# Kernel tuning notes

Measured on AMD Instinct MI355X. Metric: run time of the kernel, lower is better.

The kernel has to match this reference:

```python
import jax, jax.numpy as jnp
import numpy as np

H, W, C = 512, 512, 21
D_BI, D_SP = 5, 2
THETA_ALPHA, THETA_BETA, THETA_GAMMA = 80.0, 13.0, 3.0
BILATERAL_COMPAT, SPATIAL_COMPAT, COMPAT = 10.0, 3.0, -1.0
NUM_ITER = 5


def _build_lattice(feats):
    # Permutohedral lattice construction (Adams et al. 2010), vectorized numpy.
    # feats: [N, d] float64 -> (offsets [N,d+1] int32 into M lattice points,
    # barycentric weights [N,d+1] float32, blur_neighbors [d+1, M, 2] int32 (+1, 0=missing)).
    N, d = feats.shape
    scale = (np.sqrt(2.0 / 3.0) * (d + 1)) / np.sqrt((np.arange(d) + 1.0) * (np.arange(d) + 2.0))
    cf = feats * scale                                            # [N, d]
    S = np.concatenate([np.cumsum(cf[:, ::-1], axis=1)[:, ::-1], np.zeros((N, 1))], axis=1)
    elev = np.empty((N, d + 1))
    elev[:, 0] = S[:, 0]
    elev[:, 1:] = S[:, 1:] - np.arange(1, d + 1) * cf             # embed on H_d hyperplane
    rem0 = np.floor(elev / (d + 1) + 0.5) * (d + 1)               # nearest 0-colored point
    sums = np.rint(rem0.sum(1) / (d + 1)).astype(np.int64)
    diff = elev - rem0
    idx = np.arange(d + 1)
    gt = diff[:, None, :] > diff[:, :, None]
    eq = (diff[:, None, :] == diff[:, :, None]) & (idx[None, None, :] < idx[None, :, None])
    rank = (gt | eq).sum(2).astype(np.int64) + sums[:, None]
    lo = rank < 0
    rank += (d + 1) * lo
    rem0 += (d + 1) * lo
    hi = rank > d
    rank -= (d + 1) * hi
    rem0 -= (d + 1) * hi
    v = (elev - rem0) / (d + 1)
    b = np.zeros((N, d + 2))
    rows = np.arange(N)[:, None]
    np.add.at(b, (rows, d - rank), v)
    np.add.at(b, (rows, d + 1 - rank), -v)
    b[:, 0] += 1.0 + b[:, d + 1]
    ws = b[:, :d + 1].astype(np.float32)                          # weight per remainder r
    rem0i = np.rint(rem0[:, :d]).astype(np.int64)
    r = np.arange(d + 1)
    keys = rem0i[:, None, :] + r[None, :, None] - (d + 1) * (rank[:, None, :d] > (d - r)[None, :, None])
    uniq, os_flat = np.unique(keys.reshape(-1, d), axis=0, return_inverse=True)
    M = uniq.shape[0]
    os_ = os_flat.reshape(N, d + 1).astype(np.int32)
    n1 = np.repeat(uniq[None] + 1, d + 1, axis=0)                 # [d+1, M, d]
    n2 = np.repeat(uniq[None] - 1, d + 1, axis=0)
    for j in range(d):
        n1[j, :, j] = uniq[:, j] - d
        n2[j, :, j] = uniq[:, j] + d
    allk = np.concatenate([uniq, n1.reshape(-1, d), n2.reshape(-1, d)], axis=0)
    _, inv = np.unique(allk, axis=0, return_inverse=True)
    lut = np.full(int(inv.max()) + 1, -1, np.int64)
    lut[inv[:M]] = np.arange(M)
    i1 = lut[inv[M:M + (d + 1) * M]].reshape(d + 1, M)
    i2 = lut[inv[M + (d + 1) * M:]].reshape(d + 1, M)
    bn = (np.stack([i1, i2], axis=-1) + 1).astype(np.int32)       # 0 == missing neighbor
    return os_, ws, bn


def setup_inputs():
    key = jax.random.key(0)
    k1, k2 = jax.random.split(key)
    unary = jax.random.normal(k1, (H, W, C), jnp.float32)
    # piecewise-constant random image (realistic local color coherence)
    base = np.asarray(jax.random.uniform(k2, (32, 32, 3)), dtype=np.float64) * 255.0
    image = np.kron(base, np.ones((H // 32, W // 32, 1)))
    yy, xx = np.mgrid[0:H, 0:W].astype(np.float64)
    bi = np.concatenate([np.stack([xx / THETA_ALPHA, yy / THETA_ALPHA], -1),
                         image / THETA_BETA], axis=-1).reshape(-1, D_BI)
    sp = np.stack([xx / THETA_GAMMA, yy / THETA_GAMMA], -1).reshape(-1, D_SP)
    os_b, ws_b, bn_b = _build_lattice(bi)
    os_s, ws_s, bn_s = _build_lattice(sp)
    return {'unary': unary,
            'ws_b': jnp.asarray(ws_b), 'ws_s': jnp.asarray(ws_s),
            'os_b': jnp.asarray(os_b), 'os_s': jnp.asarray(os_s),
            'bn_b': jnp.asarray(bn_b), 'bn_s': jnp.asarray(bn_s)}


def _filter(Q, os_, ws, bn, alpha):
    # splat -> blur -> slice over one permutohedral lattice
    M = bn.shape[1]
    vals = jnp.zeros((M + 1, Q.shape[-1]), Q.dtype)
    vals = vals.at[os_ + 1].add(ws[:, :, None] * Q[:, None, :])   # splat (row 0 = pad)
    for j in range(bn.shape[0]):                                  # blur along d+1 lattice axes
        vals = vals.at[1:].add(0.5 * (vals[bn[j, :, 0]] + vals[bn[j, :, 1]]))
    return alpha * jnp.einsum('nj,njc->nc', ws, vals[os_ + 1])    # slice


def reference(unary, ws_b, ws_s, os_b, os_s, bn_b, bn_s):
    U = unary.reshape(-1, unary.shape[-1])                        # [N, C]
    a_b = 1.0 / (1.0 + 2.0 ** (-D_BI))
    a_s = 1.0 / (1.0 + 2.0 ** (-D_SP))
    ones = jnp.ones((U.shape[0], 1), U.dtype)
    inv_nb = 1.0 / (_filter(ones, os_b, ws_b, bn_b, a_b) + 1e-20)
    inv_ns = 1.0 / (_filter(ones, os_s, ws_s, bn_s, a_s) + 1e-20)
    Q = jax.nn.softmax(-U, axis=-1)
    for _ in range(NUM_ITER):
        msg = BILATERAL_COMPAT * (_filter(Q, os_b, ws_b, bn_b, a_b) * inv_nb) \
            + SPATIAL_COMPAT * (_filter(Q, os_s, ws_s, bn_s, a_s) * inv_ns)
        Q = jax.nn.softmax(-U - COMPAT * msg, axis=-1)
    return Q.reshape(unary.shape)
```

## Files before the change

kernel.cpp:

```cpp
#include <hip/hip_runtime.h>
#include <hip/hip_fp16.h>

#define NCH 21
#define NCH2 22
#define VSH 32
#define QSH 32
#define USH 24
#define NPIX (512*512)
#define SEG 192
#define DECODE (1.0f/(16383.f*128.f))

__device__ __forceinline__ int wave_rank_atomic(int m, bool valid, int* __restrict__ cur) {
  int lane = threadIdx.x & 63;
  unsigned long long todo = __ballot(valid);
  int out = 0;
  while (todo) {
    int leader = __ffsll((unsigned long long)todo) - 1;
    int lm = __shfl(m, leader);
    unsigned long long match = __ballot(valid && (m == lm));
    int cnt = __popcll(match);
    int b = 0;
    if (lane == leader) b = atomicAdd(&cur[lm], cnt);
    b = __shfl(b, leader);
    if (valid && (m == lm)) out = b + __popcll(match & ((1ull << lane) - 1ull));
    todo &= ~match;
  }
  return out;
}


__global__ void count_fused_kernel(const int* __restrict__ os_b, const int* __restrict__ os_s,
                                   int* __restrict__ cnt, int nptot, int Mb) {
  int t = blockIdx.x*blockDim.x + threadIdx.x;
  bool valid = (t < nptot);
  int m = 0;
  if (valid) {
    if (t < 6*NPIX) { int j = t >> 18, n = t & (NPIX-1); m = os_b[n*6+j]; }
    else { int t2 = t - 6*NPIX; int j = t2 >> 18, n = t2 & (NPIX-1); m = Mb + os_s[n*3+j]; }
  }
  int lane = threadIdx.x & 63;
  unsigned long long todo = __ballot(valid);
  while (todo) {
    int leader = __ffsll((unsigned long long)todo) - 1;
    int lm = __shfl(m, leader);
    unsigned long long match = __ballot(valid && (m == lm));
    if (lane == leader) atomicAdd(&cnt[lm], __popcll(match));
    todo &= ~match;
  }
}

__global__ void scan_block_kernel(const int* __restrict__ cnt, int* __restrict__ excl,
                                  int* __restrict__ bsum, int M) {
  __shared__ int s[256];
  int i = blockIdx.x*256 + threadIdx.x;
  int v = (i < M) ? cnt[i] : 0;
  s[threadIdx.x] = v;
  __syncthreads();
  for (int off = 1; off < 256; off <<= 1) {
    int t = (threadIdx.x >= off) ? s[threadIdx.x - off] : 0;
    __syncthreads();
    s[threadIdx.x] += t;
    __syncthreads();
  }
  if (i < M) excl[i] = s[threadIdx.x] - v;
  if (threadIdx.x == 255) bsum[blockIdx.x] = s[255];
}

__global__ void scan_sums_kernel(int* __restrict__ bsum, int nb) {
  __shared__ int s[256];
  __shared__ int carry;
  if (threadIdx.x == 0) carry = 0;
  __syncthreads();
  for (int base = 0; base < nb; base += 256) {
    int i = base + threadIdx.x;
    int v = (i < nb) ? bsum[i] : 0;
    s[threadIdx.x] = v;
    __syncthreads();
    for (int off = 1; off < 256; off <<= 1) {
      int t = (threadIdx.x >= off) ? s[threadIdx.x - off] : 0;
      __syncthreads();
      s[threadIdx.x] += t;
      __syncthreads();
    }
    if (i < nb) bsum[i] = s[threadIdx.x] - v + carry;
    int tot = s[255];
    __syncthreads();
    if (threadIdx.x == 0) carry += tot;
    __syncthreads();
  }
  if (threadIdx.x == 0) bsum[nb] = carry;
}

__global__ void scan_add_kernel(int* __restrict__ excl, const int* __restrict__ bsum,
                                int M, int nb) {
  int i = blockIdx.x*blockDim.x + threadIdx.x;
  if (i < M) excl[i] += bsum[i >> 8];
  else if (i == M) excl[M] = bsum[nb];
}

__global__ void fill_fused_kernel(const int* __restrict__ os_b, const float* __restrict__ ws_b,
                                  const int* __restrict__ os_s, const float* __restrict__ ws_s,
                                  const int* __restrict__ start, int* __restrict__ cur,
                                  unsigned int* __restrict__ pw, int nptot, int Mb) {
  int t = blockIdx.x*blockDim.x + threadIdx.x;
  bool valid = (t < nptot);
  int m = 0, pix = 0; float w = 0.f;
  if (valid) {
    if (t < 6*NPIX) { int j = t >> 18, n = t & (NPIX-1); m = os_b[n*6+j]; pix = n; w = ws_b[n*6+j]; }
    else { int t2 = t - 6*NPIX; int j = t2 >> 18, n = t2 & (NPIX-1);
           m = Mb + os_s[n*3+j]; pix = n; w = ws_s[n*3+j]; }
  }
  int slot = wave_rank_atomic(m, valid, cur);
  if (valid) {
    int w14 = (int)(w * 16383.f + 0.5f);
    w14 = w14 < 0 ? 0 : (w14 > 16383 ? 16383 : w14);
    pw[start[m] + slot] = ((unsigned int)pix << 14) | (unsigned int)w14;
  }
}


__global__ void nseg_kernel(const int* __restrict__ start, int* __restrict__ segcnt, int Mtot) {
  int m = blockIdx.x*blockDim.x + threadIdx.x;
  if (m >= Mtot) return;
  int len = start[m+1] - start[m];
  segcnt[m] = (len + SEG - 1) / SEG;
}

__global__ void seg_fill_kernel(const int* __restrict__ segstart, int* __restrict__ seg_m, int Mtot) {
  int m = blockIdx.x*blockDim.x + threadIdx.x;
  if (m >= Mtot) return;
  int b = segstart[m], e = segstart[m+1];
  for (int s = b; s < e; ++s) seg_m[s] = m;
}


__global__ void gather_seg_kernel(const __half* __restrict__ Qh, const int* __restrict__ start,
                                  const int* __restrict__ segstart, const int* __restrict__ seg_m,
                                  const unsigned int* __restrict__ pw,
                                  float* __restrict__ partials, int Mtot) {
  int wid = blockIdx.x*(blockDim.x >> 6) + (threadIdx.x >> 6);
  int NSEG = segstart[Mtot];
  if (wid >= NSEG) return;
  int m = seg_m[wid];
  int k0 = start[m] + (wid - segstart[m])*SEG;
  int k1 = start[m+1];
  if (k1 > k0 + SEG) k1 = k0 + SEG;
  int lane = threadIdx.x & 63;
  int pg = lane / 21;
  int c  = lane - pg*21;
  float s = 0.f, wsum = 0.f;
  if (pg < 3) {
    int k = k0 + pg;
    for (; k + 9 < k1; k += 12) {
      unsigned int a0 = pw[k], a1 = pw[k+3], a2 = pw[k+6], a3 = pw[k+9];
      float w0 = (float)(a0 & 16383u), w1 = (float)(a1 & 16383u);
      float w2 = (float)(a2 & 16383u), w3 = (float)(a3 & 16383u);
      s += w0 * __half2float(Qh[((size_t)(a0 >> 14) << 5) + c])
         + w1 * __half2float(Qh[((size_t)(a1 >> 14) << 5) + c])
         + w2 * __half2float(Qh[((size_t)(a2 >> 14) << 5) + c])
         + w3 * __half2float(Qh[((size_t)(a3 >> 14) << 5) + c]);
      wsum += w0 + w1 + w2 + w3;
    }
    for (; k < k1; k += 3) {
      unsigned int a = pw[k];
      float w = (float)(a & 16383u);
      s += w * __half2float(Qh[((size_t)(a >> 14) << 5) + c]);
      wsum += w;
    }
  }
  float s1 = __shfl(s, (lane + 21) & 63);
  float s2 = __shfl(s, (lane + 42) & 63);
  float wt = __shfl(wsum, 0) + __shfl(wsum, 21) + __shfl(wsum, 42);
  float* row = partials + (size_t)wid*NCH2;
  if (lane < 21)       row[c]  = s + s1 + s2;
  else if (lane == 21) row[21] = wt;
}

__global__ void combine_kernel(const float* __restrict__ partials,
                               const int* __restrict__ segstart,
                               __half* __restrict__ valsB, __half* __restrict__ valsS,
                               int Mb, int Mtot) {
  int t = blockIdx.x*blockDim.x + threadIdx.x;
  if (t >= Mtot*NCH2) return;
  int m = t / NCH2, c = t - m*NCH2;
  int s0 = segstart[m], s1 = segstart[m+1];
  float acc = 0.f;
  int s = s0;
  for (; s + 3 < s1; s += 4)
    acc += partials[(size_t)s*NCH2+c] + partials[(size_t)(s+1)*NCH2+c]
         + partials[(size_t)(s+2)*NCH2+c] + partials[(size_t)(s+3)*NCH2+c];
  for (; s < s1; ++s) acc += partials[(size_t)s*NCH2+c];
  __half* row = (m < Mb) ? (valsB + (size_t)(m+1)*VSH) : (valsS + (size_t)(m-Mb+1)*VSH);
  row[c] = __float2half(acc * DECODE);
}

__global__ void blurH_fused_kernel(const __half* __restrict__ inB, __half* __restrict__ outB,
                                   const int* __restrict__ bnB, int Mb,
                                   const __half* __restrict__ inS, __half* __restrict__ outS,
                                   const int* __restrict__ bnS, int Ms) {
  int t = blockIdx.x*blockDim.x + threadIdx.x;
  const __half* in; __half* out; const int* bn; int i, j;
  int tb = Mb*11;
  if (t < tb) { i = t/11; j = t - i*11; in = inB; out = outB; bn = bnB; }
  else {
    int t2 = t - tb;
    if (t2 >= Ms*11) return;
    i = t2/11; j = t2 - i*11; in = inS; out = outS; bn = bnS;
  }
  int b0 = bn[2*i], b1 = bn[2*i+1];
  float2 a = __half22float2(((const __half2*)(in + (size_t)(i+1)*VSH))[j]);
  float2 x = __half22float2(((const __half2*)(in + (size_t)b0*VSH))[j]);
  float2 y = __half22float2(((const __half2*)(in + (size_t)b1*VSH))[j]);
  float2 o;
  o.x = a.x + 0.5f*(x.x + y.x);
  o.y = a.y + 0.5f*(x.y + y.y);
  ((__half2*)(out + (size_t)(i+1)*VSH))[j] = __float22half2_rn(o);
}


__global__ void softmax_init_kernel(const float* __restrict__ U, __half* __restrict__ Qh,
                                    __half* __restrict__ Uh) {
  int n = blockIdx.x*blockDim.x + threadIdx.x;
  if (n >= NPIX) return;
  float l[NCH];
  float m = -3.4e38f;
  #pragma unroll
  for (int c = 0; c < NCH; ++c) {
    l[c] = -U[(size_t)n*NCH+c];
    Uh[(size_t)n*USH+c] = __float2half(l[c]);
    m = fmaxf(m, l[c]);
  }
  float s = 0.f;
  #pragma unroll
  for (int c = 0; c < NCH; ++c) { l[c] = expf(l[c]-m); s += l[c]; }
  float r = 1.0f/s;
  #pragma unroll
  for (int c = 0; c < NCH; ++c) Qh[(size_t)n*QSH+c] = __float2half(l[c]*r);
}

template<bool FINAL>
__global__ void slice_combine_softmax_kernel(
    const __half* __restrict__ Uh,
    const __half* __restrict__ vb, const __half* __restrict__ vs,
    const float* __restrict__ ws_b, const int* __restrict__ os_b,
    const float* __restrict__ ws_s, const int* __restrict__ os_s,
    float* __restrict__ QoutF, __half* __restrict__ QoutH) {
  int n = blockIdx.x*blockDim.x + threadIdx.x;
  if (n >= NPIX) return;
  float l[NCH];
  #pragma unroll
  for (int c = 0; c < NCH; ++c) l[c] = __half2float(Uh[(size_t)n*USH+c]);
  float acc[NCH2];
  #pragma unroll
  for (int c = 0; c < NCH2; ++c) acc[c] = 0.f;
  #pragma unroll
  for (int j = 0; j < 6; ++j) {
    float w = ws_b[n*6+j];
    const __half* v = vb + (size_t)(os_b[n*6+j]+1)*VSH;
    #pragma unroll
    for (int c = 0; c < NCH2; ++c) acc[c] += w*__half2float(v[c]);
  }
  float rb = 10.0f/(acc[NCH] + 1e-12f);
  #pragma unroll
  for (int c = 0; c < NCH; ++c) l[c] += rb*acc[c];
  #pragma unroll
  for (int c = 0; c < NCH2; ++c) acc[c] = 0.f;
  #pragma unroll
  for (int j = 0; j < 3; ++j) {
    float w = ws_s[n*3+j];
    const __half* v = vs + (size_t)(os_s[n*3+j]+1)*VSH;
    #pragma unroll
    for (int c = 0; c < NCH2; ++c) acc[c] += w*__half2float(v[c]);
  }
  float rs = 3.0f/(acc[NCH] + 1e-12f);
  #pragma unroll
  for (int c = 0; c < NCH; ++c) l[c] += rs*acc[c];
  float m = -3.4e38f;
  #pragma unroll
  for (int c = 0; c < NCH; ++c) m = fmaxf(m, l[c]);
  float s = 0.f;
  #pragma unroll
  for (int c = 0; c < NCH; ++c) { l[c] = expf(l[c]-m); s += l[c]; }
  float r = 1.0f/s;
  if (FINAL) {
    #pragma unroll
    for (int c = 0; c < NCH; ++c) QoutF[(size_t)n*NCH+c] = l[c]*r;
  } else {
    #pragma unroll
    for (int c = 0; c < NCH; ++c) QoutH[(size_t)n*QSH+c] = __float2half(l[c]*r);
  }
}


extern "C" void kernel_launch(void* const* d_in, const int* in_sizes, int n_in,
                              void* d_out, int out_size, void* d_ws, size_t ws_size,
                              hipStream_t stream) {
  const float* U    = (const float*)d_in[0];
  const float* ws_b = (const float*)d_in[1];
  const float* ws_s = (const float*)d_in[2];
  const int*   os_b = (const int*)d_in[3];
  const int*   os_s = (const int*)d_in[4];
  const int*   bn_b = (const int*)d_in[5];
  const int*   bn_s = (const int*)d_in[6];
  const int Mb = in_sizes[5] / 12;
  const int Ms = in_sizes[6] / 6;
  const int Mtot = Mb + Ms;
  const int nptot = NPIX*9;
  const int nseg_max = Mtot + nptot/SEG + 2;

  char* wcur = (char*)d_ws;
  auto alloc = [&](size_t bytes) -> void* {
    void* p = (void*)wcur;
    wcur += (bytes + 63) & ~(size_t)63;
    return p;
  };
  __half* Qh     = (__half*)alloc((size_t)NPIX*QSH*2);
  __half* Uh     = (__half*)alloc((size_t)NPIX*USH*2);
  __half* vAb    = (__half*)alloc((size_t)(Mb+1)*VSH*2);
  __half* vBb    = (__half*)alloc((size_t)(Mb+1)*VSH*2);
  __half* vAs    = (__half*)alloc((size_t)(Ms+1)*VSH*2);
  __half* vBs    = (__half*)alloc((size_t)(Ms+1)*VSH*2);
  int*   start   = (int*)alloc((size_t)(Mtot+1)*4);
  int*   cur     = (int*)alloc((size_t)Mtot*4);
  int*   segstart= (int*)alloc((size_t)(Mtot+1)*4);
  int*   seg_m   = (int*)alloc((size_t)nseg_max*4);
  unsigned int* pw = (unsigned int*)alloc((size_t)nptot*4);
  float* partials= (float*)alloc((size_t)nseg_max*NCH2*4);
  int*   bsum    = (int*)alloc((size_t)(Mtot/256 + 3)*4);

  const int TB = 256;
  auto blocks = [](long long n){ return (int)((n + 255)/256); };
  const int nbM = blocks(Mtot);

  hipMemsetAsync(cur, 0, (size_t)Mtot*sizeof(int), stream);
  count_fused_kernel<<<blocks(nptot), TB, 0, stream>>>(os_b, os_s, cur, nptot, Mb);
  scan_block_kernel<<<nbM, 256, 0, stream>>>(cur, start, bsum, Mtot);
  scan_sums_kernel<<<1, 256, 0, stream>>>(bsum, nbM);
  scan_add_kernel<<<blocks(Mtot+1), TB, 0, stream>>>(start, bsum, Mtot, nbM);
  hipMemsetAsync(cur, 0, (size_t)Mtot*sizeof(int), stream);
  fill_fused_kernel<<<blocks(nptot), TB, 0, stream>>>(os_b, ws_b, os_s, ws_s,
                                                      start, cur, pw, nptot, Mb);

  nseg_kernel<<<nbM, TB, 0, stream>>>(start, cur, Mtot);
  scan_block_kernel<<<nbM, 256, 0, stream>>>(cur, segstart, bsum, Mtot);
  scan_sums_kernel<<<1, 256, 0, stream>>>(bsum, nbM);
  scan_add_kernel<<<blocks(Mtot+1), TB, 0, stream>>>(segstart, bsum, Mtot, nbM);
  seg_fill_kernel<<<nbM, TB, 0, stream>>>(segstart, seg_m, Mtot);

  hipMemsetAsync(vAb, 0, VSH*2, stream);
  hipMemsetAsync(vBb, 0, VSH*2, stream);
  hipMemsetAsync(vAs, 0, VSH*2, stream);
  hipMemsetAsync(vBs, 0, VSH*2, stream);

  softmax_init_kernel<<<blocks(NPIX), TB, 0, stream>>>(U, Qh, Uh);

  for (int it = 0; it < 5; ++it) {
    gather_seg_kernel<<<blocks((long long)nseg_max*64), TB, 0, stream>>>(
        Qh, start, segstart, seg_m, pw, partials, Mtot);
    combine_kernel<<<blocks((long long)Mtot*NCH2), TB, 0, stream>>>(
        partials, segstart, vAb, vAs, Mb, Mtot);
    __half* ab = vAb; __half* bb = vBb;
    __half* as = vAs; __half* bs = vBs;
    for (int j = 0; j < 6; ++j) {
      int ms = (j < 3) ? Ms : 0;
      blurH_fused_kernel<<<blocks((long long)(Mb + ms)*11), TB, 0, stream>>>(
          ab, bb, bn_b + (size_t)j*Mb*2, Mb, as, bs, bn_s + (size_t)j*Ms*2, ms);
      { __half* t = ab; ab = bb; bb = t; }
      if (j < 3) { __half* t = as; as = bs; bs = t; }
    }
    if (it == 4) {
      slice_combine_softmax_kernel<true><<<blocks(NPIX), TB, 0, stream>>>(
          Uh, ab, as, ws_b, os_b, ws_s, os_s, (float*)d_out, (__half*)nullptr);
    } else {
      slice_combine_softmax_kernel<false><<<blocks(NPIX), TB, 0, stream>>>(
          Uh, ab, as, ws_b, os_b, ws_s, os_s, (float*)nullptr, Qh);
    }
  }
}
```

Before: 531.9 us.

## Replace segmented gather+combine with one-wave-per-vertex gather and packed slice entries

Drops the segment decomposition (nseg, scan, seg_fill), the partials buffer and the combine kernel, so each wave gathers a whole lattice vertex and writes half-precision values directly. It also precomputes a packed slice array of 12-bit weights and vertex offsets laid out by remainder index, giving coalesced single loads in the slice kernel. This removes several launches and a partials round trip, but loses load balancing for vertices with long splat lists and lowers slice weight precision to 12 bits.

```diff
diff --git a/kernel.cpp b/kernel.cpp
--- a/kernel.cpp
+++ b/kernel.cpp
@@ -7,7 +7,6 @@
 #define QSH 32
 #define USH 24
 #define NPIX (512*512)
-#define SEG 192
 #define DECODE (1.0f/(16383.f*128.f))
 
 __device__ __forceinline__ int wave_rank_atomic(int m, bool valid, int* __restrict__ cur) {
@@ -118,39 +117,33 @@
   }
 }
 
-
-__global__ void nseg_kernel(const int* __restrict__ start, int* __restrict__ segcnt, int Mtot) {
-  int m = blockIdx.x*blockDim.x + threadIdx.x;
-  if (m >= Mtot) return;
-  int len = start[m+1] - start[m];
-  segcnt[m] = (len + SEG - 1) / SEG;
-}
-
-__global__ void seg_fill_kernel(const int* __restrict__ segstart, int* __restrict__ seg_m, int Mtot) {
-  int m = blockIdx.x*blockDim.x + threadIdx.x;
-  if (m >= Mtot) return;
-  int b = segstart[m], e = segstart[m+1];
-  for (int s = b; s < e; ++s) seg_m[s] = m;
-}
-
-
-__global__ void gather_seg_kernel(const __half* __restrict__ Qh, const int* __restrict__ start,
-                                  const int* __restrict__ segstart, const int* __restrict__ seg_m,
-                                  const unsigned int* __restrict__ pw,
-                                  float* __restrict__ partials, int Mtot) {
+__global__ void pack_slice_kernel(const int* __restrict__ os_b, const float* __restrict__ ws_b,
+                                  const int* __restrict__ os_s, const float* __restrict__ ws_s,
+                                  unsigned int* __restrict__ sl, int nptot) {
+  int t = blockIdx.x*blockDim.x + threadIdx.x;
+  if (t >= nptot) return;
+  int o; float w;
+  if (t < 6*NPIX) { int j = t >> 18, n = t & (NPIX-1); o = os_b[n*6+j] + 1; w = ws_b[n*6+j]; }
+  else { int t2 = t - 6*NPIX; int j = t2 >> 18, n = t2 & (NPIX-1); o = os_s[n*3+j] + 1; w = ws_s[n*3+j]; }
+  int w12 = (int)(w * 4095.f + 0.5f);
+  w12 = w12 < 0 ? 0 : (w12 > 4095 ? 4095 : w12);
+  sl[t] = ((unsigned int)o << 12) | (unsigned int)w12;
+}
+
+
+__global__ void gather_wave_kernel(const __half* __restrict__ Qh, const int* __restrict__ start,
+                                   const unsigned int* __restrict__ pw,
+                                   __half* __restrict__ valsB, __half* __restrict__ valsS,
+                                   int Mb, int Mtot) {
   int wid = blockIdx.x*(blockDim.x >> 6) + (threadIdx.x >> 6);
-  int NSEG = segstart[Mtot];
-  if (wid >= NSEG) return;
-  int m = seg_m[wid];
-  int k0 = start[m] + (wid - segstart[m])*SEG;
-  int k1 = start[m+1];
-  if (k1 > k0 + SEG) k1 = k0 + SEG;
+  if (wid >= Mtot) return;
   int lane = threadIdx.x & 63;
   int pg = lane / 21;
   int c  = lane - pg*21;
   float s = 0.f, wsum = 0.f;
+  int k1 = start[wid+1];
   if (pg < 3) {
-    int k = k0 + pg;
+    int k = start[wid] + pg;
     for (; k + 9 < k1; k += 12) {
       unsigned int a0 = pw[k], a1 = pw[k+3], a2 = pw[k+6], a3 = pw[k+9];
       float w0 = (float)(a0 & 16383u), w1 = (float)(a1 & 16383u);
@@ -171,27 +164,10 @@
   float s1 = __shfl(s, (lane + 21) & 63);
   float s2 = __shfl(s, (lane + 42) & 63);
   float wt = __shfl(wsum, 0) + __shfl(wsum, 21) + __shfl(wsum, 42);
-  float* row = partials + (size_t)wid*NCH2;
-  if (lane < 21)       row[c]  = s + s1 + s2;
-  else if (lane == 21) row[21] = wt;
-}
-
-__global__ void combine_kernel(const float* __restrict__ partials,
-                               const int* __restrict__ segstart,
-                               __half* __restrict__ valsB, __half* __restrict__ valsS,
-                               int Mb, int Mtot) {
-  int t = blockIdx.x*blockDim.x + threadIdx.x;
-  if (t >= Mtot*NCH2) return;
-  int m = t / NCH2, c = t - m*NCH2;
-  int s0 = segstart[m], s1 = segstart[m+1];
-  float acc = 0.f;
-  int s = s0;
-  for (; s + 3 < s1; s += 4)
-    acc += partials[(size_t)s*NCH2+c] + partials[(size_t)(s+1)*NCH2+c]
-         + partials[(size_t)(s+2)*NCH2+c] + partials[(size_t)(s+3)*NCH2+c];
-  for (; s < s1; ++s) acc += partials[(size_t)s*NCH2+c];
-  __half* row = (m < Mb) ? (valsB + (size_t)(m+1)*VSH) : (valsS + (size_t)(m-Mb+1)*VSH);
-  row[c] = __float2half(acc * DECODE);
+  __half* row = (wid < Mb) ? (valsB + (size_t)(wid+1)*VSH)
+                           : (valsS + (size_t)(wid-Mb+1)*VSH);
+  if (lane < 21)       row[c]  = __float2half((s + s1 + s2) * DECODE);
+  else if (lane == 21) row[21] = __float2half(wt * DECODE);
 }
 
 __global__ void blurH_fused_kernel(const __half* __restrict__ inB, __half* __restrict__ outB,
@@ -238,10 +214,11 @@
   for (int c = 0; c < NCH; ++c) Qh[(size_t)n*QSH+c] = __float2half(l[c]*r);
 }
 
-template<bool FINAL>
+template<bool FINAL, bool PACKED>
 __global__ void slice_combine_softmax_kernel(
     const __half* __restrict__ Uh,
     const __half* __restrict__ vb, const __half* __restrict__ vs,
+    const unsigned int* __restrict__ sl,
     const float* __restrict__ ws_b, const int* __restrict__ os_b,
     const float* __restrict__ ws_s, const int* __restrict__ os_s,
     float* __restrict__ QoutF, __half* __restrict__ QoutH) {
@@ -255,8 +232,15 @@
   for (int c = 0; c < NCH2; ++c) acc[c] = 0.f;
   #pragma unroll
   for (int j = 0; j < 6; ++j) {
-    float w = ws_b[n*6+j];
-    const __half* v = vb + (size_t)(os_b[n*6+j]+1)*VSH;
+    float w; const __half* v;
+    if (PACKED) {
+      unsigned int e = sl[(size_t)j*NPIX + n];
+      w = (float)(e & 4095u);
+      v = vb + ((size_t)(e >> 12) << 5);
+    } else {
+      w = ws_b[n*6+j];
+      v = vb + (size_t)(os_b[n*6+j]+1)*VSH;
+    }
     #pragma unroll
     for (int c = 0; c < NCH2; ++c) acc[c] += w*__half2float(v[c]);
   }
@@ -267,8 +251,15 @@
   for (int c = 0; c < NCH2; ++c) acc[c] = 0.f;
   #pragma unroll
   for (int j = 0; j < 3; ++j) {
-    float w = ws_s[n*3+j];
-    const __half* v = vs + (size_t)(os_s[n*3+j]+1)*VSH;
+    float w; const __half* v;
+    if (PACKED) {
+      unsigned int e = sl[(size_t)(6+j)*NPIX + n];
+      w = (float)(e & 4095u);
+      v = vs + ((size_t)(e >> 12) << 5);
+    } else {
+      w = ws_s[n*3+j];
+      v = vs + (size_t)(os_s[n*3+j]+1)*VSH;
+    }
     #pragma unroll
     for (int c = 0; c < NCH2; ++c) acc[c] += w*__half2float(v[c]);
   }
@@ -306,7 +297,7 @@
   const int Ms = in_sizes[6] / 6;
   const int Mtot = Mb + Ms;
   const int nptot = NPIX*9;
-  const int nseg_max = Mtot + nptot/SEG + 2;
+  const bool packed = (Mtot + 1) < (1 << 20);
 
   char* wcur = (char*)d_ws;
   auto alloc = [&](size_t bytes) -> void* {
@@ -322,10 +313,8 @@
   __half* vBs    = (__half*)alloc((size_t)(Ms+1)*VSH*2);
   int*   start   = (int*)alloc((size_t)(Mtot+1)*4);
   int*   cur     = (int*)alloc((size_t)Mtot*4);
-  int*   segstart= (int*)alloc((size_t)(Mtot+1)*4);
-  int*   seg_m   = (int*)alloc((size_t)nseg_max*4);
   unsigned int* pw = (unsigned int*)alloc((size_t)nptot*4);
-  float* partials= (float*)alloc((size_t)nseg_max*NCH2*4);
+  unsigned int* sl = (unsigned int*)alloc((size_t)nptot*4);
   int*   bsum    = (int*)alloc((size_t)(Mtot/256 + 3)*4);
 
   const int TB = 256;
@@ -340,12 +329,8 @@
   hipMemsetAsync(cur, 0, (size_t)Mtot*sizeof(int), stream);
   fill_fused_kernel<<<blocks(nptot), TB, 0, stream>>>(os_b, ws_b, os_s, ws_s,
                                                       start, cur, pw, nptot, Mb);
-
-  nseg_kernel<<<nbM, TB, 0, stream>>>(start, cur, Mtot);
-  scan_block_kernel<<<nbM, 256, 0, stream>>>(cur, segstart, bsum, Mtot);
-  scan_sums_kernel<<<1, 256, 0, stream>>>(bsum, nbM);
-  scan_add_kernel<<<blocks(Mtot+1), TB, 0, stream>>>(segstart, bsum, Mtot, nbM);
-  seg_fill_kernel<<<nbM, TB, 0, stream>>>(segstart, seg_m, Mtot);
+  if (packed)
+    pack_slice_kernel<<<blocks(nptot), TB, 0, stream>>>(os_b, ws_b, os_s, ws_s, sl, nptot);
 
   hipMemsetAsync(vAb, 0, VSH*2, stream);
   hipMemsetAsync(vBb, 0, VSH*2, stream);
@@ -355,10 +340,8 @@
   softmax_init_kernel<<<blocks(NPIX), TB, 0, stream>>>(U, Qh, Uh);
 
   for (int it = 0; it < 5; ++it) {
-    gather_seg_kernel<<<blocks((long long)nseg_max*64), TB, 0, stream>>>(
-        Qh, start, segstart, seg_m, pw, partials, Mtot);
-    combine_kernel<<<blocks((long long)Mtot*NCH2), TB, 0, stream>>>(
-        partials, segstart, vAb, vAs, Mb, Mtot);
+    gather_wave_kernel<<<blocks((long long)Mtot*64), TB, 0, stream>>>(
+        Qh, start, pw, vAb, vAs, Mb, Mtot);
     __half* ab = vAb; __half* bb = vBb;
     __half* as = vAs; __half* bs = vBs;
     for (int j = 0; j < 6; ++j) {
@@ -369,11 +352,19 @@
       if (j < 3) { __half* t = as; as = bs; bs = t; }
     }
     if (it == 4) {
-      slice_combine_softmax_kernel<true><<<blocks(NPIX), TB, 0, stream>>>(
-          Uh, ab, as, ws_b, os_b, ws_s, os_s, (float*)d_out, (__half*)nullptr);
+      if (packed)
+        slice_combine_softmax_kernel<true,true><<<blocks(NPIX), TB, 0, stream>>>(
+            Uh, ab, as, sl, ws_b, os_b, ws_s, os_s, (float*)d_out, (__half*)nullptr);
+      else
+        slice_combine_softmax_kernel<true,false><<<blocks(NPIX), TB, 0, stream>>>(
+            Uh, ab, as, sl, ws_b, os_b, ws_s, os_s, (float*)d_out, (__half*)nullptr);
     } else {
-      slice_combine_softmax_kernel<false><<<blocks(NPIX), TB, 0, stream>>>(
-          Uh, ab, as, ws_b, os_b, ws_s, os_s, (float*)nullptr, Qh);
-    }
-  }
-}
+      if (packed)
+        slice_combine_softmax_kernel<false,true><<<blocks(NPIX), TB, 0, stream>>>(
+            Uh, ab, as, sl, ws_b, os_b, ws_s, os_s, (float*)nullptr, Qh);
+      else
+        slice_combine_softmax_kernel<false,false><<<blocks(NPIX), TB, 0, stream>>>(
+            Uh, ab, as, sl, ws_b, os_b, ws_s, os_s, (float*)nullptr, Qh);
+    }
+  }
+}
```

After: 484.4 us. -8.9%, faster.
